# Kernel tuning notes

Hardware: AMD Instinct MI355X
Metric: run time of the kernel (lower is better)

Reference implementation:

```python
import jax, jax.numpy as jnp
import numpy as np

NV, NC = 100000, 50000        # num variables, num constraints
DV, DC = 8, 16                # padded neighbor-list widths
DIN, DH = 32, 128             # init_input_dim, output_dim (=init_output_dim)
NUM_LAYERS = 3                # aggregate loop runs num_layers-1 times
DCAT = 2 * DH + DIN           # input_dim of fc_variable/fc_constraint


def setup_inputs() -> dict:
    key = jax.random.key(0)
    ks = jax.random.split(key, 10)
    w = lambda k, shape: (jax.random.normal(k, shape, jnp.float32) * 0.05)
    return {
        "x": jax.random.normal(ks[0], (NV + NC, DIN), jnp.float32),
        "var_constr_index": jax.random.randint(ks[1], (NV, DV), 0, NC, dtype=jnp.int32),
        "constr_var_index": jax.random.randint(ks[2], (NC, DC), 0, NV, dtype=jnp.int32),
        "W_init_v": w(ks[3], (DIN, DH)), "b_init_v": jnp.zeros((DH,), jnp.float32),
        "W_init_c": w(ks[4], (DIN, DH)), "b_init_c": jnp.zeros((DH,), jnp.float32),
        "W_var": w(ks[5], (DCAT, DH)), "b_var": jnp.zeros((DH,), jnp.float32),
        "W_con": w(ks[6], (DCAT, DH)), "b_con": jnp.zeros((DH,), jnp.float32),
        "W_q": w(ks[7], (2 * DH, 1)), "b_q": jnp.zeros((1,), jnp.float32),
    }


def reference(x, var_constr_index, constr_var_index,
              W_init_v, b_init_v, W_init_c, b_init_c,
              W_var, b_var, W_con, b_con, W_q, b_q):
    nv = var_constr_index.shape[0]
    xv, xc = x[:nv], x[nv:]
    # layer zero init (fc_init_variables / fc_init_constraints)
    v = xv @ W_init_v + b_init_v          # [NV, DH]
    c = xc @ W_init_c + b_init_c          # [NC, DH]
    # message-passing layers: both updates read OLD v and OLD c
    for _ in range(1, NUM_LAYERS):
        agg_c = jnp.sum(v[constr_var_index], axis=1)   # [NC, DH] gather+sum over variable neighbors
        agg_v = jnp.sum(c[var_constr_index], axis=1)   # [NV, DH] gather+sum over constraint neighbors
        c_new = jnp.concatenate([agg_c, c, xc], axis=1) @ W_con + b_con
        v_new = jnp.concatenate([agg_v, v, xv], axis=1) @ W_var + b_var
        c, v = c_new, v_new
    # embedding_Q: global sum of variable features, broadcast, concat, linear
    g = jnp.sum(v, axis=0)                             # [DH]
    q_in = jnp.concatenate([jnp.broadcast_to(g, v.shape), v], axis=1)  # [NV, 2*DH]
    return q_in @ W_q + b_q                            # [NV, 1]
```

## Files before the change

### kernel.cpp

```cpp
#include <hip/hip_runtime.h>

#define NV 100000
#define NC 50000
#define DVAR 8
#define DCON 16

using short8 = __attribute__((ext_vector_type(8))) short;
using f32x4  = __attribute__((ext_vector_type(4))) float;

__device__ __forceinline__ unsigned short f2bf(float f) {
    union { float f; unsigned int u; } v; v.f = f;
    return (unsigned short)((v.u + 0x7fffu + ((v.u >> 16) & 1u)) >> 16);
}
__device__ __forceinline__ float bflo(unsigned int u) {
    union { unsigned int u; float f; } v; v.u = u << 16; return v.f;
}
__device__ __forceinline__ float bfhi(unsigned int u) {
    union { unsigned int u; float f; } v; v.u = u & 0xffff0000u; return v.f;
}

__global__ __launch_bounds__(256) void pack_kernel(
    const float* __restrict__ Wvar, const float* __restrict__ Wcon,
    const float* __restrict__ Wiv,  const float* __restrict__ Wic,
    unsigned short* __restrict__ WbVar, unsigned short* __restrict__ WbCon,
    unsigned short* __restrict__ WbIv,  unsigned short* __restrict__ WbIc,
    float* __restrict__ S)
{
    const int tid = blockIdx.x * 256 + threadIdx.x;
    for (int i = tid; i < 9 * 128 * 32; i += gridDim.x * 256) {
        int s = i >> 12, rem = i & 4095, c = rem >> 5, k = rem & 31;
        int src = (s * 32 + k) * 128 + c;
        WbVar[i] = f2bf(Wvar[src]);
        WbCon[i] = f2bf(Wcon[src]);
    }
    for (int i = tid; i < 128 * 32; i += gridDim.x * 256) {
        int c = i >> 5, k = i & 31;
        int src = k * 128 + c;
        WbIv[i] = f2bf(Wiv[src]);
        WbIc[i] = f2bf(Wic[src]);
    }
    if (tid == 0) S[0] = 0.f;
}

__global__ __launch_bounds__(256) void init_mfma(
    const float* __restrict__ x,
    const unsigned short* __restrict__ Wb,
    const float* __restrict__ bias,
    unsigned short* __restrict__ hout, int M)
{
    const int t = threadIdx.x;
    const int lane = t & 63;
    const int w = t >> 6;
    const int lrow = lane & 15;
    const int lg = lane >> 4;
    const int wrow0 = blockIdx.x * 64 + w * 16;
    int arow = wrow0 + lrow;
    int arowc = arow < M ? arow : M - 1;

    const float4* xp = (const float4*)(x + (size_t)arowc * 32 + lg * 8);
    float4 xa = xp[0], xb = xp[1];
    short8 afr;
    afr[0] = (short)f2bf(xa.x); afr[1] = (short)f2bf(xa.y);
    afr[2] = (short)f2bf(xa.z); afr[3] = (short)f2bf(xa.w);
    afr[4] = (short)f2bf(xb.x); afr[5] = (short)f2bf(xb.y);
    afr[6] = (short)f2bf(xb.z); afr[7] = (short)f2bf(xb.w);

    #pragma unroll
    for (int ct = 0; ct < 8; ++ct) {
        int c = ct * 16 + lrow;
        short8 bfr = *(const short8*)(Wb + (size_t)c * 32 + lg * 8);
        f32x4 acc = {0.f, 0.f, 0.f, 0.f};
        acc = __builtin_amdgcn_mfma_f32_16x16x32_bf16(afr, bfr, acc, 0, 0, 0);
        float bv = bias[c];
        #pragma unroll
        for (int r = 0; r < 4; ++r) {
            int orow = wrow0 + lg * 4 + r;
            if (orow < M) hout[(size_t)orow * 128 + c] = f2bf(acc[r] + bv);
        }
    }
}

template<int DEG, bool FINAL>
__global__ __launch_bounds__(256) void layer_mfma(
    const unsigned short* hself,
    const unsigned short* __restrict__ hnb,
    const float* __restrict__ xself,
    const int* __restrict__ idx,
    const unsigned short* __restrict__ Wb,
    const float* __restrict__ bias,
    unsigned short* hout,
    const float* __restrict__ Wq, float* __restrict__ S, float* __restrict__ dotout,
    int M)
{
    __shared__ float red[4];
    const int t = threadIdx.x;
    const int lane = t & 63;
    const int w = t >> 6;
    const int lrow = lane & 15;
    const int lg = lane >> 4;
    const int wrow0 = blockIdx.x * 64 + w * 16;
    const int arow = wrow0 + lrow;
    const int arowc = arow < M ? arow : M - 1;

    int nb[DEG];
    #pragma unroll
    for (int d4 = 0; d4 < DEG / 4; ++d4)
        *(int4*)(&nb[d4 * 4]) = *(const int4*)(idx + (size_t)arowc * DEG + d4 * 4);

    short8 sfr[4];
    #pragma unroll
    for (int s = 0; s < 4; ++s)
        sfr[s] = *(const short8*)(hself + (size_t)arowc * 128 + s * 32 + lg * 8);
    short8 xfr;
    {
        const float4* xp = (const float4*)(xself + (size_t)arowc * 32 + lg * 8);
        float4 xa = xp[0], xb = xp[1];
        xfr[0] = (short)f2bf(xa.x); xfr[1] = (short)f2bf(xa.y);
        xfr[2] = (short)f2bf(xa.z); xfr[3] = (short)f2bf(xa.w);
        xfr[4] = (short)f2bf(xb.x); xfr[5] = (short)f2bf(xb.y);
        xfr[6] = (short)f2bf(xb.z); xfr[7] = (short)f2bf(xb.w);
    }

    float ag[4][8];
    #pragma unroll
    for (int s = 0; s < 4; ++s)
        #pragma unroll
        for (int j = 0; j < 8; ++j) ag[s][j] = 0.f;
    #pragma unroll
    for (int d = 0; d < DEG; ++d) {
        const unsigned short* rp = hnb + (size_t)nb[d] * 128 + lg * 8;
        #pragma unroll
        for (int s = 0; s < 4; ++s) {
            const uint4 q = *(const uint4*)(rp + s * 32);
            ag[s][0] += bflo(q.x); ag[s][1] += bfhi(q.x);
            ag[s][2] += bflo(q.y); ag[s][3] += bfhi(q.y);
            ag[s][4] += bflo(q.z); ag[s][5] += bfhi(q.z);
            ag[s][6] += bflo(q.w); ag[s][7] += bfhi(q.w);
        }
    }

    f32x4 acc[8];
    #pragma unroll
    for (int ct = 0; ct < 8; ++ct) acc[ct] = (f32x4){0.f, 0.f, 0.f, 0.f};

    #pragma unroll
    for (int s = 4; s < 9; ++s) {
        short8 afr = (s < 8) ? sfr[s - 4] : xfr;
        #pragma unroll
        for (int ct = 0; ct < 8; ++ct) {
            short8 bfr = *(const short8*)(Wb + ((size_t)s * 128 + ct * 16 + lrow) * 32 + lg * 8);
            acc[ct] = __builtin_amdgcn_mfma_f32_16x16x32_bf16(afr, bfr, acc[ct], 0, 0, 0);
        }
    }
    #pragma unroll
    for (int s = 0; s < 4; ++s) {
        short8 afr;
        #pragma unroll
        for (int j = 0; j < 8; ++j) afr[j] = (short)f2bf(ag[s][j]);
        #pragma unroll
        for (int ct = 0; ct < 8; ++ct) {
            short8 bfr = *(const short8*)(Wb + ((size_t)s * 128 + ct * 16 + lrow) * 32 + lg * 8);
            acc[ct] = __builtin_amdgcn_mfma_f32_16x16x32_bf16(afr, bfr, acc[ct], 0, 0, 0);
        }
    }

    if (!FINAL) {
        #pragma unroll
        for (int ct = 0; ct < 8; ++ct) {
            int c = ct * 16 + lrow;
            float bv = bias[c];
            #pragma unroll
            for (int r = 0; r < 4; ++r) {
                int orow = wrow0 + lg * 4 + r;
                if (orow < M) hout[(size_t)orow * 128 + c] = f2bf(acc[ct][r] + bv);
            }
        }
    } else {
        float d0[4] = {0.f, 0.f, 0.f, 0.f};
        float d1[4] = {0.f, 0.f, 0.f, 0.f};
        #pragma unroll
        for (int ct = 0; ct < 8; ++ct) {
            int c = ct * 16 + lrow;
            float bv = bias[c];
            float wq0 = Wq[c];
            float wq1 = Wq[128 + c];
            #pragma unroll
            for (int r = 0; r < 4; ++r) {
                int orow = wrow0 + lg * 4 + r;
                float val = (orow < M) ? (acc[ct][r] + bv) : 0.f;
                d0[r] += val * wq0;
                d1[r] += val * wq1;
            }
        }
        #pragma unroll
        for (int r = 0; r < 4; ++r) {
            d0[r] += __shfl_xor(d0[r], 1); d0[r] += __shfl_xor(d0[r], 2);
            d0[r] += __shfl_xor(d0[r], 4); d0[r] += __shfl_xor(d0[r], 8);
            d1[r] += __shfl_xor(d1[r], 1); d1[r] += __shfl_xor(d1[r], 2);
            d1[r] += __shfl_xor(d1[r], 4); d1[r] += __shfl_xor(d1[r], 8);
        }
        if (lrow == 0) {
            #pragma unroll
            for (int r = 0; r < 4; ++r) {
                int orow = wrow0 + lg * 4 + r;
                if (orow < M) dotout[orow] = d1[r];
            }
        }
        float tot = d0[0] + d0[1] + d0[2] + d0[3];
        tot += __shfl_xor(tot, 16);
        tot += __shfl_xor(tot, 32);
        if (lane == 0) red[w] = tot;
        __syncthreads();
        if (t == 0) atomicAdd(S, red[0] + red[1] + red[2] + red[3]);
    }
}

__global__ __launch_bounds__(256) void addout_kernel(
    float* __restrict__ outp, const float* __restrict__ S,
    const float* __restrict__ bq, int n)
{
    int i = blockIdx.x * 256 + threadIdx.x;
    if (i < n) outp[i] = outp[i] + S[0] + bq[0];
}

extern "C" void kernel_launch(void* const* d_in, const int* in_sizes, int n_in,
                              void* d_out, int out_size, void* d_ws, size_t ws_size,
                              hipStream_t stream)
{
    const float* x    = (const float*)d_in[0];
    const int*   vci  = (const int*)  d_in[1];
    const int*   cvi  = (const int*)  d_in[2];
    const float* Wiv  = (const float*)d_in[3];
    const float* biv  = (const float*)d_in[4];
    const float* Wic  = (const float*)d_in[5];
    const float* bic  = (const float*)d_in[6];
    const float* Wvar = (const float*)d_in[7];
    const float* bvar = (const float*)d_in[8];
    const float* Wcon = (const float*)d_in[9];
    const float* bcon = (const float*)d_in[10];
    const float* Wq   = (const float*)d_in[11];
    const float* bq   = (const float*)d_in[12];
    float* outp = (float*)d_out;

    unsigned short* us = (unsigned short*)d_ws;
    size_t o = 0;
    unsigned short* vA    = us + o; o += (size_t)NV * 128;
    unsigned short* cA    = us + o; o += (size_t)NC * 128;
    unsigned short* cB    = us + o; o += (size_t)NC * 128;
    unsigned short* WbVar = us + o; o += 9 * 128 * 32;
    unsigned short* WbCon = us + o; o += 9 * 128 * 32;
    unsigned short* WbIv  = us + o; o += 128 * 32;
    unsigned short* WbIc  = us + o; o += 128 * 32;
    float* S = (float*)(us + o);

    const float* xc = x + (size_t)NV * 32;

    pack_kernel<<<144, 256, 0, stream>>>(Wvar, Wcon, Wiv, Wic, WbVar, WbCon, WbIv, WbIc, S);
    init_mfma<<<(NV + 63) / 64, 256, 0, stream>>>(x,  WbIv, biv, vA, NV);
    init_mfma<<<(NC + 63) / 64, 256, 0, stream>>>(xc, WbIc, bic, cA, NC);
    layer_mfma<DCON, false><<<(NC + 63) / 64, 256, 0, stream>>>(
        cA, vA, xc, cvi, WbCon, bcon, cB, nullptr, nullptr, nullptr, NC);
    layer_mfma<DVAR, false><<<(NV + 63) / 64, 256, 0, stream>>>(
        vA, cA, x, vci, WbVar, bvar, vA, nullptr, nullptr, nullptr, NV);
    layer_mfma<DVAR, true><<<(NV + 63) / 64, 256, 0, stream>>>(
        vA, cB, x, vci, WbVar, bvar, nullptr, Wq, S, outp, NV);
    addout_kernel<<<(NV + 255) / 256, 256, 0, stream>>>(outp, S, bq, NV);
}
```

Before: 313.4 us.

## Split neighbor aggregation into separate gather kernel before MFMA GEMM

The fused gather-plus-GEMM layer kernel is split into a dedicated aggregation kernel, with 16 threads per row and 8 neighbor loads in flight each, that writes bf16 sums to new workspace buffers. A separate MFMA GEMM kernel then reads those sums alongside the self features and inputs. The aim is more memory-level parallelism in the random gathers and lower register pressure in the GEMM. The cost is an extra round trip of the aggregated features through global memory plus two more launches.

```diff
diff --git a/kernel.cpp b/kernel.cpp
--- a/kernel.cpp
+++ b/kernel.cpp
@@ -80,12 +80,47 @@
     }
 }
 
-template<int DEG, bool FINAL>
-__global__ __launch_bounds__(256) void layer_mfma(
+template<int DEG>
+__global__ __launch_bounds__(256) void agg_bf16(
+    const unsigned short* __restrict__ hnb, const int* __restrict__ idx,
+    unsigned short* __restrict__ agg, int M)
+{
+    const int tid = blockIdx.x * 256 + threadIdx.x;
+    const int row = tid >> 4;
+    const int part = tid & 15;
+    if (row >= M) return;
+    int nb[DEG];
+    #pragma unroll
+    for (int d4 = 0; d4 < DEG / 4; ++d4)
+        *(int4*)(&nb[d4 * 4]) = *(const int4*)(idx + (size_t)row * DEG + d4 * 4);
+    float a0=0.f,a1=0.f,a2=0.f,a3=0.f,a4=0.f,a5=0.f,a6=0.f,a7=0.f;
+    #pragma unroll
+    for (int b = 0; b < DEG; b += 8) {
+        uint4 q[8];
+        #pragma unroll
+        for (int j = 0; j < 8; ++j)
+            q[j] = *(const uint4*)(hnb + (size_t)nb[b + j] * 128 + part * 8);
+        #pragma unroll
+        for (int j = 0; j < 8; ++j) {
+            a0 += bflo(q[j].x); a1 += bfhi(q[j].x);
+            a2 += bflo(q[j].y); a3 += bfhi(q[j].y);
+            a4 += bflo(q[j].z); a5 += bfhi(q[j].z);
+            a6 += bflo(q[j].w); a7 += bfhi(q[j].w);
+        }
+    }
+    uint4 o;
+    o.x = (unsigned)f2bf(a0) | ((unsigned)f2bf(a1) << 16);
+    o.y = (unsigned)f2bf(a2) | ((unsigned)f2bf(a3) << 16);
+    o.z = (unsigned)f2bf(a4) | ((unsigned)f2bf(a5) << 16);
+    o.w = (unsigned)f2bf(a6) | ((unsigned)f2bf(a7) << 16);
+    *(uint4*)(agg + (size_t)row * 128 + part * 8) = o;
+}
+
+template<bool FINAL>
+__global__ __launch_bounds__(256) void gemm_mfma(
     const unsigned short* hself,
-    const unsigned short* __restrict__ hnb,
+    const unsigned short* __restrict__ aggin,
     const float* __restrict__ xself,
-    const int* __restrict__ idx,
     const unsigned short* __restrict__ Wb,
     const float* __restrict__ bias,
     unsigned short* hout,
@@ -102,41 +137,22 @@
     const int arow = wrow0 + lrow;
     const int arowc = arow < M ? arow : M - 1;
 
-    int nb[DEG];
-    #pragma unroll
-    for (int d4 = 0; d4 < DEG / 4; ++d4)
-        *(int4*)(&nb[d4 * 4]) = *(const int4*)(idx + (size_t)arowc * DEG + d4 * 4);
-
-    short8 sfr[4];
+    short8 afr[9];
     #pragma unroll
     for (int s = 0; s < 4; ++s)
-        sfr[s] = *(const short8*)(hself + (size_t)arowc * 128 + s * 32 + lg * 8);
-    short8 xfr;
+        afr[s] = *(const short8*)(aggin + (size_t)arowc * 128 + s * 32 + lg * 8);
+    #pragma unroll
+    for (int s = 0; s < 4; ++s)
+        afr[4 + s] = *(const short8*)(hself + (size_t)arowc * 128 + s * 32 + lg * 8);
     {
         const float4* xp = (const float4*)(xself + (size_t)arowc * 32 + lg * 8);
         float4 xa = xp[0], xb = xp[1];
+        short8 xfr;
         xfr[0] = (short)f2bf(xa.x); xfr[1] = (short)f2bf(xa.y);
         xfr[2] = (short)f2bf(xa.z); xfr[3] = (short)f2bf(xa.w);
         xfr[4] = (short)f2bf(xb.x); xfr[5] = (short)f2bf(xb.y);
         xfr[6] = (short)f2bf(xb.z); xfr[7] = (short)f2bf(xb.w);
-    }
-
-    float ag[4][8];
-    #pragma unroll
-    for (int s = 0; s < 4; ++s)
-        #pragma unroll
-        for (int j = 0; j < 8; ++j) ag[s][j] = 0.f;
-    #pragma unroll
-    for (int d = 0; d < DEG; ++d) {
-        const unsigned short* rp = hnb + (size_t)nb[d] * 128 + lg * 8;
-        #pragma unroll
-        for (int s = 0; s < 4; ++s) {
-            const uint4 q = *(const uint4*)(rp + s * 32);
-            ag[s][0] += bflo(q.x); ag[s][1] += bfhi(q.x);
-            ag[s][2] += bflo(q.y); ag[s][3] += bfhi(q.y);
-            ag[s][4] += bflo(q.z); ag[s][5] += bfhi(q.z);
-            ag[s][6] += bflo(q.w); ag[s][7] += bfhi(q.w);
-        }
+        afr[8] = xfr;
     }
 
     f32x4 acc[8];
@@ -144,23 +160,11 @@
     for (int ct = 0; ct < 8; ++ct) acc[ct] = (f32x4){0.f, 0.f, 0.f, 0.f};
 
     #pragma unroll
-    for (int s = 4; s < 9; ++s) {
-        short8 afr = (s < 8) ? sfr[s - 4] : xfr;
+    for (int s = 0; s < 9; ++s) {
         #pragma unroll
         for (int ct = 0; ct < 8; ++ct) {
             short8 bfr = *(const short8*)(Wb + ((size_t)s * 128 + ct * 16 + lrow) * 32 + lg * 8);
-            acc[ct] = __builtin_amdgcn_mfma_f32_16x16x32_bf16(afr, bfr, acc[ct], 0, 0, 0);
-        }
-    }
-    #pragma unroll
-    for (int s = 0; s < 4; ++s) {
-        short8 afr;
-        #pragma unroll
-        for (int j = 0; j < 8; ++j) afr[j] = (short)f2bf(ag[s][j]);
-        #pragma unroll
-        for (int ct = 0; ct < 8; ++ct) {
-            short8 bfr = *(const short8*)(Wb + ((size_t)s * 128 + ct * 16 + lrow) * 32 + lg * 8);
-            acc[ct] = __builtin_amdgcn_mfma_f32_16x16x32_bf16(afr, bfr, acc[ct], 0, 0, 0);
+            acc[ct] = __builtin_amdgcn_mfma_f32_16x16x32_bf16(afr[s], bfr, acc[ct], 0, 0, 0);
         }
     }
 
@@ -247,6 +251,8 @@
     unsigned short* vA    = us + o; o += (size_t)NV * 128;
     unsigned short* cA    = us + o; o += (size_t)NC * 128;
     unsigned short* cB    = us + o; o += (size_t)NC * 128;
+    unsigned short* aggV  = us + o; o += (size_t)NV * 128;
+    unsigned short* aggC  = us + o; o += (size_t)NC * 128;
     unsigned short* WbVar = us + o; o += 9 * 128 * 32;
     unsigned short* WbCon = us + o; o += 9 * 128 * 32;
     unsigned short* WbIv  = us + o; o += 128 * 32;
@@ -258,11 +264,17 @@
     pack_kernel<<<144, 256, 0, stream>>>(Wvar, Wcon, Wiv, Wic, WbVar, WbCon, WbIv, WbIc, S);
     init_mfma<<<(NV + 63) / 64, 256, 0, stream>>>(x,  WbIv, biv, vA, NV);
     init_mfma<<<(NC + 63) / 64, 256, 0, stream>>>(xc, WbIc, bic, cA, NC);
-    layer_mfma<DCON, false><<<(NC + 63) / 64, 256, 0, stream>>>(
-        cA, vA, xc, cvi, WbCon, bcon, cB, nullptr, nullptr, nullptr, NC);
-    layer_mfma<DVAR, false><<<(NV + 63) / 64, 256, 0, stream>>>(
-        vA, cA, x, vci, WbVar, bvar, vA, nullptr, nullptr, nullptr, NV);
-    layer_mfma<DVAR, true><<<(NV + 63) / 64, 256, 0, stream>>>(
-        vA, cB, x, vci, WbVar, bvar, nullptr, Wq, S, outp, NV);
+
+    agg_bf16<DCON><<<(NC * 16 + 255) / 256, 256, 0, stream>>>(vA, cvi, aggC, NC);
+    agg_bf16<DVAR><<<(NV * 16 + 255) / 256, 256, 0, stream>>>(cA, vci, aggV, NV);
+    gemm_mfma<false><<<(NC + 63) / 64, 256, 0, stream>>>(
+        cA, aggC, xc, WbCon, bcon, cB, nullptr, nullptr, nullptr, NC);
+    gemm_mfma<false><<<(NV + 63) / 64, 256, 0, stream>>>(
+        vA, aggV, x, WbVar, bvar, vA, nullptr, nullptr, nullptr, NV);
+
+    agg_bf16<DVAR><<<(NV * 16 + 255) / 256, 256, 0, stream>>>(cB, vci, aggV, NV);
+    gemm_mfma<true><<<(NV + 63) / 64, 256, 0, stream>>>(
+        vA, aggV, x, WbVar, bvar, nullptr, Wq, S, outp, NV);
+
     addout_kernel<<<(NV + 255) / 256, 256, 0, stream>>>(outp, S, bq, NV);
 }
```

After: 303.7 us. -3.1%, faster.

## Stage weights and gathered aggregates in LDS, pre-pack x to bf16

Applied to the files above, without the earlier changes.

The layer kernel now loads the first 8 weight slices into shared memory with direct global-to-LDS loads. The neighbour gather is restructured so each thread handles one 16-byte slice for four rows, and the bf16 aggregate tile is written to swizzled LDS before the MFMA loop. A separate kernel converts x to bf16 once, so the layer kernels read packed bf16 instead of converting floats themselves. The goal is fewer redundant global weight reads and more memory-level parallelism in the gather. In exchange it uses about 80KB of LDS per block, which limits occupancy, and adds an extra kernel launch.

```diff
diff --git a/kernel.cpp b/kernel.cpp
--- a/kernel.cpp
+++ b/kernel.cpp
@@ -7,6 +7,9 @@
 
 using short8 = __attribute__((ext_vector_type(8))) short;
 using f32x4  = __attribute__((ext_vector_type(4))) float;
+
+typedef const __attribute__((address_space(1))) void* as1cv;
+typedef __attribute__((address_space(3))) void* as3v;
 
 __device__ __forceinline__ unsigned short f2bf(float f) {
     union { float f; unsigned int u; } v; v.f = f;
@@ -40,6 +43,21 @@
         WbIc[i] = f2bf(Wic[src]);
     }
     if (tid == 0) S[0] = 0.f;
+}
+
+__global__ __launch_bounds__(256) void xpack_kernel(
+    const float* __restrict__ x, unsigned short* __restrict__ xb, int n8)
+{
+    int i = blockIdx.x * 256 + threadIdx.x;
+    if (i >= n8) return;
+    const float4* p = (const float4*)(x + (size_t)i * 8);
+    float4 a = p[0], b = p[1];
+    uint4 o;
+    o.x = (unsigned)f2bf(a.x) | ((unsigned)f2bf(a.y) << 16);
+    o.y = (unsigned)f2bf(a.z) | ((unsigned)f2bf(a.w) << 16);
+    o.z = (unsigned)f2bf(b.x) | ((unsigned)f2bf(b.y) << 16);
+    o.w = (unsigned)f2bf(b.z) | ((unsigned)f2bf(b.w) << 16);
+    *(uint4*)(xb + (size_t)i * 8) = o;
 }
 
 __global__ __launch_bounds__(256) void init_mfma(
@@ -81,10 +99,10 @@
 }
 
 template<int DEG, bool FINAL>
-__global__ __launch_bounds__(256) void layer_mfma(
+__global__ __launch_bounds__(256, 2) void layer_fused(
     const unsigned short* hself,
     const unsigned short* __restrict__ hnb,
-    const float* __restrict__ xself,
+    const unsigned short* __restrict__ xb,
     const int* __restrict__ idx,
     const unsigned short* __restrict__ Wb,
     const float* __restrict__ bias,
@@ -92,77 +110,107 @@
     const float* __restrict__ Wq, float* __restrict__ S, float* __restrict__ dotout,
     int M)
 {
-    __shared__ float red[4];
+    __shared__ __align__(16) unsigned short Bs[8 * 128 * 32];
+    __shared__ __align__(16) unsigned short As[64 * 128];
     const int t = threadIdx.x;
     const int lane = t & 63;
     const int w = t >> 6;
     const int lrow = lane & 15;
     const int lg = lane >> 4;
-    const int wrow0 = blockIdx.x * 64 + w * 16;
+    const int r0 = blockIdx.x * 64;
+
+    #pragma unroll
+    for (int i = 0; i < 16; ++i) {
+        int chunk = i * 256 + t;
+        __builtin_amdgcn_global_load_lds((as1cv)(Wb + (size_t)chunk * 8),
+                                         (as3v)(Bs + (size_t)chunk * 8), 16, 0, 0);
+    }
+
+    {
+        const int slice = t & 15;
+        const int rbase = t >> 4;
+        float ac[4][8];
+        #pragma unroll
+        for (int p = 0; p < 4; ++p)
+            #pragma unroll
+            for (int j = 0; j < 8; ++j) ac[p][j] = 0.f;
+
+        #pragma unroll
+        for (int h = 0; h < DEG; h += 8) {
+            int nb8[4][8];
+            #pragma unroll
+            for (int p = 0; p < 4; ++p) {
+                int row = r0 + p * 16 + rbase;
+                int rowc = row < M ? row : M - 1;
+                *(int4*)&nb8[p][0] = *(const int4*)(idx + (size_t)rowc * DEG + h);
+                *(int4*)&nb8[p][4] = *(const int4*)(idx + (size_t)rowc * DEG + h + 4);
+            }
+            uint4 q[4][8];
+            #pragma unroll
+            for (int p = 0; p < 4; ++p)
+                #pragma unroll
+                for (int j = 0; j < 8; ++j)
+                    q[p][j] = *(const uint4*)(hnb + (size_t)nb8[p][j] * 128 + slice * 8);
+            #pragma unroll
+            for (int p = 0; p < 4; ++p)
+                #pragma unroll
+                for (int j = 0; j < 8; ++j) {
+                    ac[p][0] += bflo(q[p][j].x); ac[p][1] += bfhi(q[p][j].x);
+                    ac[p][2] += bflo(q[p][j].y); ac[p][3] += bfhi(q[p][j].y);
+                    ac[p][4] += bflo(q[p][j].z); ac[p][5] += bfhi(q[p][j].z);
+                    ac[p][6] += bflo(q[p][j].w); ac[p][7] += bfhi(q[p][j].w);
+                }
+        }
+        #pragma unroll
+        for (int p = 0; p < 4; ++p) {
+            int rl = p * 16 + rbase;
+            int cs = slice ^ (rl & 7);
+            uint4 o;
+            o.x = (unsigned)f2bf(ac[p][0]) | ((unsigned)f2bf(ac[p][1]) << 16);
+            o.y = (unsigned)f2bf(ac[p][2]) | ((unsigned)f2bf(ac[p][3]) << 16);
+            o.z = (unsigned)f2bf(ac[p][4]) | ((unsigned)f2bf(ac[p][5]) << 16);
+            o.w = (unsigned)f2bf(ac[p][6]) | ((unsigned)f2bf(ac[p][7]) << 16);
+            *(uint4*)(As + ((size_t)rl * 16 + cs) * 8) = o;
+        }
+    }
+    __syncthreads();
+
+    const int wrow0 = r0 + w * 16;
     const int arow = wrow0 + lrow;
     const int arowc = arow < M ? arow : M - 1;
 
-    int nb[DEG];
-    #pragma unroll
-    for (int d4 = 0; d4 < DEG / 4; ++d4)
-        *(int4*)(&nb[d4 * 4]) = *(const int4*)(idx + (size_t)arowc * DEG + d4 * 4);
-
     short8 sfr[4];
     #pragma unroll
-    for (int s = 0; s < 4; ++s)
-        sfr[s] = *(const short8*)(hself + (size_t)arowc * 128 + s * 32 + lg * 8);
-    short8 xfr;
-    {
-        const float4* xp = (const float4*)(xself + (size_t)arowc * 32 + lg * 8);
-        float4 xa = xp[0], xb = xp[1];
-        xfr[0] = (short)f2bf(xa.x); xfr[1] = (short)f2bf(xa.y);
-        xfr[2] = (short)f2bf(xa.z); xfr[3] = (short)f2bf(xa.w);
-        xfr[4] = (short)f2bf(xb.x); xfr[5] = (short)f2bf(xb.y);
-        xfr[6] = (short)f2bf(xb.z); xfr[7] = (short)f2bf(xb.w);
-    }
-
-    float ag[4][8];
-    #pragma unroll
-    for (int s = 0; s < 4; ++s)
-        #pragma unroll
-        for (int j = 0; j < 8; ++j) ag[s][j] = 0.f;
-    #pragma unroll
-    for (int d = 0; d < DEG; ++d) {
-        const unsigned short* rp = hnb + (size_t)nb[d] * 128 + lg * 8;
-        #pragma unroll
-        for (int s = 0; s < 4; ++s) {
-            const uint4 q = *(const uint4*)(rp + s * 32);
-            ag[s][0] += bflo(q.x); ag[s][1] += bfhi(q.x);
-            ag[s][2] += bflo(q.y); ag[s][3] += bfhi(q.y);
-            ag[s][4] += bflo(q.z); ag[s][5] += bfhi(q.z);
-            ag[s][6] += bflo(q.w); ag[s][7] += bfhi(q.w);
-        }
-    }
+    for (int s4 = 0; s4 < 4; ++s4)
+        sfr[s4] = *(const short8*)(hself + (size_t)arowc * 128 + s4 * 32 + lg * 8);
+    short8 xfr = *(const short8*)(xb + (size_t)arowc * 32 + lg * 8);
+    short8 b8[8];
+    #pragma unroll
+    for (int ct = 0; ct < 8; ++ct)
+        b8[ct] = *(const short8*)(Wb + ((size_t)8 * 128 + ct * 16 + lrow) * 32 + lg * 8);
 
     f32x4 acc[8];
     #pragma unroll
     for (int ct = 0; ct < 8; ++ct) acc[ct] = (f32x4){0.f, 0.f, 0.f, 0.f};
 
     #pragma unroll
-    for (int s = 4; s < 9; ++s) {
-        short8 afr = (s < 8) ? sfr[s - 4] : xfr;
+    for (int s = 0; s < 8; ++s) {
+        short8 afr;
+        if (s < 4) {
+            int chunk = (4 * s + lg) ^ (lrow & 7);
+            afr = *(const short8*)(As + ((size_t)(w * 16 + lrow) * 16 + chunk) * 8);
+        } else {
+            afr = sfr[s - 4];
+        }
         #pragma unroll
         for (int ct = 0; ct < 8; ++ct) {
-            short8 bfr = *(const short8*)(Wb + ((size_t)s * 128 + ct * 16 + lrow) * 32 + lg * 8);
+            short8 bfr = *(const short8*)(Bs + ((size_t)s * 128 + ct * 16 + lrow) * 32 + lg * 8);
             acc[ct] = __builtin_amdgcn_mfma_f32_16x16x32_bf16(afr, bfr, acc[ct], 0, 0, 0);
         }
     }
     #pragma unroll
-    for (int s = 0; s < 4; ++s) {
-        short8 afr;
-        #pragma unroll
-        for (int j = 0; j < 8; ++j) afr[j] = (short)f2bf(ag[s][j]);
-        #pragma unroll
-        for (int ct = 0; ct < 8; ++ct) {
-            short8 bfr = *(const short8*)(Wb + ((size_t)s * 128 + ct * 16 + lrow) * 32 + lg * 8);
-            acc[ct] = __builtin_amdgcn_mfma_f32_16x16x32_bf16(afr, bfr, acc[ct], 0, 0, 0);
-        }
-    }
+    for (int ct = 0; ct < 8; ++ct)
+        acc[ct] = __builtin_amdgcn_mfma_f32_16x16x32_bf16(xfr, b8[ct], acc[ct], 0, 0, 0);
 
     if (!FINAL) {
         #pragma unroll
@@ -209,6 +257,8 @@
         float tot = d0[0] + d0[1] + d0[2] + d0[3];
         tot += __shfl_xor(tot, 16);
         tot += __shfl_xor(tot, 32);
+        __syncthreads();
+        float* red = (float*)As;
         if (lane == 0) red[w] = tot;
         __syncthreads();
         if (t == 0) atomicAdd(S, red[0] + red[1] + red[2] + red[3]);
@@ -247,6 +297,7 @@
     unsigned short* vA    = us + o; o += (size_t)NV * 128;
     unsigned short* cA    = us + o; o += (size_t)NC * 128;
     unsigned short* cB    = us + o; o += (size_t)NC * 128;
+    unsigned short* xbAll = us + o; o += (size_t)(NV + NC) * 32;
     unsigned short* WbVar = us + o; o += 9 * 128 * 32;
     unsigned short* WbCon = us + o; o += 9 * 128 * 32;
     unsigned short* WbIv  = us + o; o += 128 * 32;
@@ -254,15 +305,20 @@
     float* S = (float*)(us + o);
 
     const float* xc = x + (size_t)NV * 32;
+    unsigned short* xbV = xbAll;
+    unsigned short* xbC = xbAll + (size_t)NV * 32;
 
     pack_kernel<<<144, 256, 0, stream>>>(Wvar, Wcon, Wiv, Wic, WbVar, WbCon, WbIv, WbIc, S);
+    xpack_kernel<<<((NV + NC) * 4 + 255) / 256, 256, 0, stream>>>(x, xbAll, (NV + NC) * 4);
     init_mfma<<<(NV + 63) / 64, 256, 0, stream>>>(x,  WbIv, biv, vA, NV);
     init_mfma<<<(NC + 63) / 64, 256, 0, stream>>>(xc, WbIc, bic, cA, NC);
-    layer_mfma<DCON, false><<<(NC + 63) / 64, 256, 0, stream>>>(
-        cA, vA, xc, cvi, WbCon, bcon, cB, nullptr, nullptr, nullptr, NC);
-    layer_mfma<DVAR, false><<<(NV + 63) / 64, 256, 0, stream>>>(
-        vA, cA, x, vci, WbVar, bvar, vA, nullptr, nullptr, nullptr, NV);
-    layer_mfma<DVAR, true><<<(NV + 63) / 64, 256, 0, stream>>>(
-        vA, cB, x, vci, WbVar, bvar, nullptr, Wq, S, outp, NV);
+
+    layer_fused<DCON, false><<<(NC + 63) / 64, 256, 0, stream>>>(
+        cA, vA, xbC, cvi, WbCon, bcon, cB, nullptr, nullptr, nullptr, NC);
+    layer_fused<DVAR, false><<<(NV + 63) / 64, 256, 0, stream>>>(
+        vA, cA, xbV, vci, WbVar, bvar, vA, nullptr, nullptr, nullptr, NV);
+    layer_fused<DVAR, true><<<(NV + 63) / 64, 256, 0, stream>>>(
+        vA, cB, xbV, vci, WbVar, bvar, nullptr, Wq, S, outp, NV);
+
     addout_kernel<<<(NV + 255) / 256, 256, 0, stream>>>(outp, S, bq, NV);
 }
```

After: 267.5 us. 1.17x faster.
